# Kernel tuning notes

Measured on AMD Instinct MI355X. Metric: run time of the kernel, lower is better.

The kernel has to match this reference:

```python
import jax, jax.numpy as jnp
import numpy as np

B, S, D, H = 4, 2048, 512, 8
DK = D // H


def setup_inputs() -> dict:
    key = jax.random.key(0)
    ks = jax.random.split(key, 8)
    std = 1.0 / np.sqrt(D)
    return {
        "query": jax.random.normal(ks[0], (B, S, D), jnp.float32),
        "key": jax.random.normal(ks[1], (B, S, D), jnp.float32),
        "value": jax.random.normal(ks[2], (B, S, D), jnp.float32),
        "Wq": jax.random.normal(ks[3], (D, D), jnp.float32) * std,
        "Wk": jax.random.normal(ks[4], (D, D), jnp.float32) * std,
        "Wv": jax.random.normal(ks[5], (D, D), jnp.float32) * std,
        "Wo": jax.random.normal(ks[6], (D, D), jnp.float32) * std,
        "bo": jnp.zeros((D,), jnp.float32),
    }


def reference(query, key, value, Wq, Wk, Wv, Wo, bo):
    # nn.Linear stores weight [out, in]; y = x @ W.T
    def split_heads(x):  # [B,S,D] -> [B,H,S,DK]
        return x.reshape(B, S, H, DK).transpose(0, 2, 1, 3)

    Q = split_heads(query @ Wq.T)
    K = split_heads(key @ Wk.T)
    V = split_heads(value @ Wv.T)
    scale = jnp.sqrt(jnp.asarray(DK, Q.dtype))
    scores = jnp.einsum("bhqd,bhkd->bhqk", Q, K) / scale  # [B,H,S,S]
    attn = jax.nn.softmax(scores, axis=-1)  # dropout=0 / eval mode
    ctx = jnp.einsum("bhqk,bhkd->bhqd", attn, V)
    ctx = ctx.transpose(0, 2, 1, 3).reshape(B, S, D)
    return ctx @ Wo.T + bo
```

## Files before the change

### kernel.cpp

```cpp
#include <hip/hip_runtime.h>
#include <hip/hip_bf16.h>
#include <stdint.h>

#define DEV __device__ __forceinline__

typedef __attribute__((ext_vector_type(8))) __bf16 bf16x8;
typedef __attribute__((ext_vector_type(4))) float f32x4;
typedef __attribute__((ext_vector_type(16))) float f32x16;
typedef __attribute__((ext_vector_type(4))) short short4v;
typedef __attribute__((ext_vector_type(8))) short short8v;
typedef __attribute__((ext_vector_type(4))) unsigned int uint4v;

constexpr int B_ = 4, S_ = 2048, D_ = 512, H_ = 8, DK_ = 64;
constexpr int M_ = B_ * S_;
constexpr int K_ = D_;

DEV unsigned short f2bf(float f) {
  unsigned int u = __builtin_bit_cast(unsigned int, f);
  unsigned int r = (u + 0x7fffu + ((u >> 16) & 1u)) >> 16;
  return (unsigned short)r;
}

DEV void gld16(const void* g, void* l) {
  __builtin_amdgcn_global_load_lds(
      (const __attribute__((address_space(1))) unsigned int*)g,
      (__attribute__((address_space(3))) unsigned int*)l, 16, 0, 0);
}

DEV f32x4 mfma16(bf16x8 a, bf16x8 b, f32x4 c) {
  return __builtin_amdgcn_mfma_f32_16x16x32_bf16(a, b, c, 0, 0, 0);
}
DEV f32x16 mfma32(bf16x8 a, bf16x8 b, f32x16 c) {
  return __builtin_amdgcn_mfma_f32_32x32x16_bf16(a, b, c, 0, 0, 0);
}

DEV short4v tr16(const void* p) {
  short4v d;
  asm volatile("ds_read_b64_tr_b16 %0, %1"
               : "=v"(d)
               : "v"((const __attribute__((address_space(3))) char*)p));
  return d;
}

DEV unsigned pkbf(float a, float b) {
  unsigned r;
  asm("v_cvt_pk_bf16_f32 %0, %1, %2" : "=v"(r) : "v"(a), "v"(b));
  return r;
}

DEV void pl32swap(unsigned& a, unsigned& b) {
  asm volatile("v_permlane32_swap_b32 %0, %1" : "+v"(a), "+v"(b));
}

__global__ __launch_bounds__(256) void convert_all(
    const float* __restrict__ q, const float* __restrict__ k, const float* __restrict__ v,
    const float* __restrict__ wq, const float* __restrict__ wk,
    const float* __restrict__ wv, const float* __restrict__ wo,
    unsigned short* __restrict__ xq, unsigned short* __restrict__ xk,
    unsigned short* __restrict__ xv, unsigned short* __restrict__ wqb,
    unsigned short* __restrict__ wkb, unsigned short* __restrict__ wvb,
    unsigned short* __restrict__ wob)
{
  constexpr int NX = M_ * D_;
  constexpr int NW = D_ * D_;
  constexpr int TOT = (3 * NX + 4 * NW) / 4;
  for (int u = blockIdx.x * blockDim.x + threadIdx.x; u < TOT;
       u += gridDim.x * blockDim.x) {
    int e = u * 4;
    const float* src; unsigned short* dst; int off;
    if (e < 3 * NX) {
      int t = e >> 22; off = e & (NX - 1);
      src = (t == 0) ? q : ((t == 1) ? k : v);
      dst = (t == 0) ? xq : ((t == 1) ? xk : xv);
    } else {
      int e2 = e - 3 * NX;
      int t = e2 >> 18; off = e2 & (NW - 1);
      src = (t == 0) ? wq : ((t == 1) ? wk : ((t == 2) ? wv : wo));
      dst = (t == 0) ? wqb : ((t == 1) ? wkb : ((t == 2) ? wvb : wob));
    }
    float4 f = *(const float4*)(src + off);
    short4v o;
    o.x = (short)f2bf(f.x); o.y = (short)f2bf(f.y);
    o.z = (short)f2bf(f.z); o.w = (short)f2bf(f.w);
    *(short4v*)(dst + off) = o;
  }
}

template <int MODE>
__global__ __launch_bounds__(256, 2) void gemm_bt(
    const unsigned short* __restrict__ A0, const unsigned short* __restrict__ A1,
    const unsigned short* __restrict__ A2,
    const unsigned short* __restrict__ W0, const unsigned short* __restrict__ W1,
    const unsigned short* __restrict__ W2,
    unsigned short* __restrict__ O0, unsigned short* __restrict__ O1,
    unsigned short* __restrict__ O2,
    float* __restrict__ outF, const float* __restrict__ bias)
{
  constexpr int BM = (MODE == 0) ? 128 : 64;
  constexpr int BN = 128, BK = 64, NKT = K_ / BK;
  constexpr int AFR = BM / 32;
  __shared__ unsigned short As[2][BM * BK];
  __shared__ unsigned short Bs[2][BN * BK];
  const int tid = threadIdx.x, lane = tid & 63, wave = tid >> 6;
  const int z = blockIdx.z;
  const unsigned short* A = (MODE == 1 || z == 0) ? A0 : (z == 1 ? A1 : A2);
  const unsigned short* W = (MODE == 1 || z == 0) ? W0 : (z == 1 ? W1 : W2);
  unsigned short* outH = (MODE == 1 || z == 0) ? O0 : (z == 1 ? O1 : O2);
  const int bn0 = blockIdx.x * BN, bm0 = blockIdx.y * BM;
  const int wr = (wave >> 1) * (BM / 2), wc = (wave & 1) * 64;
  const int frow = lane & 15, fk16 = (lane >> 4) * 16;

  f32x4 acc[AFR][4];
#pragma unroll
  for (int i = 0; i < AFR; ++i)
#pragma unroll
    for (int j = 0; j < 4; ++j)
#pragma unroll
      for (int r = 0; r < 4; ++r) acc[i][j][r] = 0.f;

  auto stage = [&](int kt, int buf) {
#pragma unroll
    for (int i = 0; i < BM / 32; ++i) {
      int o = (wave * (BM / 32) + i) * 1024;
      int ol = o + lane * 16;
      int row = ol >> 7, off = (ol ^ ((row & 7) << 4)) & 127;
      gld16((const char*)A + (size_t)(bm0 + row) * (K_ * 2) + kt * 128 + off,
            (char*)As[buf] + o);
    }
#pragma unroll
    for (int i = 0; i < 4; ++i) {
      int o = (wave * 4 + i) * 1024;
      int ol = o + lane * 16;
      int row = ol >> 7, off = (ol ^ ((row & 7) << 4)) & 127;
      gld16((const char*)W + (size_t)(bn0 + row) * (K_ * 2) + kt * 128 + off,
            (char*)Bs[buf] + o);
    }
  };

  stage(0, 0);
  __syncthreads();
  int cur = 0;
  for (int kt = 0; kt < NKT; ++kt) {
    if (kt + 1 < NKT) stage(kt + 1, cur ^ 1);
#pragma unroll
    for (int kc = 0; kc < 2; ++kc) {
      bf16x8 a[AFR], b[4];
#pragma unroll
      for (int i = 0; i < AFR; ++i) {
        int row = wr + i * 16 + frow;
        a[i] = *(const bf16x8*)((const char*)As[cur] +
                ((row * 128 + kc * 64 + fk16) ^ ((row & 7) << 4)));
      }
#pragma unroll
      for (int j = 0; j < 4; ++j) {
        int row = wc + j * 16 + frow;
        b[j] = *(const bf16x8*)((const char*)Bs[cur] +
                ((row * 128 + kc * 64 + fk16) ^ ((row & 7) << 4)));
      }
      __builtin_amdgcn_s_setprio(1);
#pragma unroll
      for (int i = 0; i < AFR; ++i)
#pragma unroll
        for (int j = 0; j < 4; ++j)
          acc[i][j] = mfma16(a[i], b[j], acc[i][j]);
      __builtin_amdgcn_s_setprio(0);
    }
    __syncthreads();
    cur ^= 1;
  }

  const int r0 = (lane >> 4) * 4, cn = lane & 15;
  float bv[4];
  if (MODE == 1) {
#pragma unroll
    for (int j = 0; j < 4; ++j) bv[j] = bias[bn0 + wc + j * 16 + cn];
  }
#pragma unroll
  for (int i = 0; i < AFR; ++i)
#pragma unroll
    for (int j = 0; j < 4; ++j)
#pragma unroll
      for (int r = 0; r < 4; ++r) {
        int gm = bm0 + wr + i * 16 + r0 + r;
        int gn = bn0 + wc + j * 16 + cn;
        float val = acc[i][j][r];
        if (MODE == 0) outH[(size_t)gm * D_ + gn] = f2bf(val);
        else           outF[(size_t)gm * D_ + gn] = val + bv[j];
      }
}

__global__ __launch_bounds__(256, 2) void attn(
    const unsigned short* __restrict__ Qm, const unsigned short* __restrict__ Km,
    const unsigned short* __restrict__ Vm, unsigned short* __restrict__ Ctx)
{
  constexpr int QB = 128, KVB = 64, NT = S_ / KVB;
  __shared__ unsigned short Qs[QB * DK_];
  __shared__ unsigned short Kd[2][KVB * DK_];
  __shared__ unsigned short Vd[2][KVB * DK_];
  __shared__ float smA[4][32];
  const int tid = threadIdx.x, lane = tid & 63, wave = tid >> 6;
  const int hi = lane >> 5, l31 = lane & 31, g1 = (lane >> 4) & 1;
  const int bh = blockIdx.y, q0 = blockIdx.x * QB;
  const int bq = bh >> 3, hh = bh & 7;
  const char* Qg = (const char*)(Qm + ((size_t)bq * S_ + q0) * D_ + hh * DK_);
  const char* Kg = (const char*)(Km + (size_t)bq * S_ * D_ + hh * DK_);
  const char* Vg = (const char*)(Vm + (size_t)bq * S_ * D_ + hh * DK_);

  auto stageSwz = [&](const char* gbase, unsigned short* lds, int o) {
    int ol = o + lane * 16;
    int row = ol >> 7, off = (ol ^ ((row & 7) << 4)) & 127;
    gld16(gbase + (size_t)row * 1024 + off, (char*)lds + o);
  };
  auto stageVt = [&](const char* gbase, unsigned short* lds, int o) {
    int ol = o + lane * 16;
    int E0 = ol >> 1;
    int st = E0 >> 6, rr = (E0 >> 4) & 3, c0 = E0 & 15;
    int kk = (st >> 2) * 4 + rr, dd = (st & 3) * 16 + c0;
    gld16(gbase + (size_t)kk * 1024 + dd * 2, (char*)lds + o);
  };

#pragma unroll
  for (int i = 0; i < 4; ++i) stageSwz(Qg, Qs, (wave * 4 + i) * 1024);
#pragma unroll
  for (int i = 0; i < 2; ++i) stageSwz(Kg, Kd[0], (wave * 2 + i) * 1024);
#pragma unroll
  for (int i = 0; i < 2; ++i) stageVt(Vg, Vd[0], (wave * 2 + i) * 1024);
  __syncthreads();

  bf16x8 qf[4];
  {
    int row = wave * 32 + l31;
    int rb = row * 128, sw = (row & 7) << 4;
#pragma unroll
    for (int c = 0; c < 4; ++c)
      qf[c] = *(const bf16x8*)((const char*)Qs + ((rb + c * 32 + hi * 16) ^ sw));
  }

  f32x16 oacc[2];
#pragma unroll
  for (int dt = 0; dt < 2; ++dt)
#pragma unroll
    for (int r = 0; r < 16; ++r) oacc[dt][r] = 0.f;
  float m2 = -1e30f, lsum = 0.f;
  constexpr float SCL2 = 0.125f * 1.44269504089f;

  int cur = 0;
  for (int t = 0; t < NT; ++t) {
    if (t + 1 < NT) {
      const char* Kg1 = Kg + (size_t)(t + 1) * KVB * 1024;
      const char* Vg1 = Vg + (size_t)(t + 1) * KVB * 1024;
#pragma unroll
      for (int i = 0; i < 2; ++i) stageSwz(Kg1, Kd[cur ^ 1], (wave * 2 + i) * 1024);
#pragma unroll
      for (int i = 0; i < 2; ++i) stageVt(Vg1, Vd[cur ^ 1], (wave * 2 + i) * 1024);
    }

    f32x16 sacc[2];
#pragma unroll
    for (int k2 = 0; k2 < 2; ++k2)
#pragma unroll
      for (int r = 0; r < 16; ++r) sacc[k2][r] = 0.f;
    __builtin_amdgcn_s_setprio(1);
#pragma unroll
    for (int c = 0; c < 4; ++c) {
#pragma unroll
      for (int k2 = 0; k2 < 2; ++k2) {
        int row = k2 * 32 + l31;
        bf16x8 kf = *(const bf16x8*)((const char*)Kd[cur] +
                     ((row * 128 + c * 32 + hi * 16) ^ ((row & 7) << 4)));
        sacc[k2] = mfma32(kf, qf[c], sacc[k2]);
      }
    }
    __builtin_amdgcn_s_setprio(0);

    float mloc = sacc[0][0];
#pragma unroll
    for (int k2 = 0; k2 < 2; ++k2)
#pragma unroll
      for (int r = 0; r < 16; ++r) mloc = fmaxf(mloc, sacc[k2][r]);
    mloc = fmaxf(mloc, __shfl_xor(mloc, 32));
    float m2n = fmaxf(m2, mloc * SCL2);
    float alpha = __builtin_amdgcn_exp2f(m2 - m2n);
    m2 = m2n;
    float psum = 0.f;
#pragma unroll
    for (int k2 = 0; k2 < 2; ++k2)
#pragma unroll
      for (int r = 0; r < 16; ++r) {
        float p = __builtin_amdgcn_exp2f(fmaf(sacc[k2][r], SCL2, -m2n));
        sacc[k2][r] = p;
        psum += p;
      }
    psum += __shfl_xor(psum, 32);
    lsum = lsum * alpha + psum;

    if (lane < 32) smA[wave][lane] = alpha;
    f32x4 av[4];
#pragma unroll
    for (int s = 0; s < 4; ++s)
      av[s] = *(const f32x4*)&smA[wave][s * 8 + hi * 4];
#pragma unroll
    for (int dt = 0; dt < 2; ++dt)
#pragma unroll
      for (int r = 0; r < 16; ++r) oacc[dt][r] *= av[r >> 2][r & 3];

    short4v va[4][2][2];
#pragma unroll
    for (int c = 0; c < 4; ++c)
#pragma unroll
      for (int dt = 0; dt < 2; ++dt) {
        int st = 16 * c + 8 * hi + 2 * dt + g1;
        const char* ad = (const char*)Vd[cur] + st * 128 + (lane & 15) * 8;
        va[c][dt][0] = tr16(ad);
        va[c][dt][1] = tr16(ad + 512);
      }
    bf16x8 pfrag[4];
#pragma unroll
    for (int c = 0; c < 4; ++c) {
      const f32x16& P = sacc[c >> 1];
      const int b = (c & 1) * 8;
      unsigned d0 = pkbf(P[b + 0], P[b + 1]);
      unsigned d1 = pkbf(P[b + 2], P[b + 3]);
      unsigned d2 = pkbf(P[b + 4], P[b + 5]);
      unsigned d3 = pkbf(P[b + 6], P[b + 7]);
      pl32swap(d0, d2);
      pl32swap(d1, d3);
      uint4v pi = {d0, d1, d2, d3};
      pfrag[c] = __builtin_bit_cast(bf16x8, pi);
    }
    asm volatile("s_waitcnt lgkmcnt(0)" ::: "memory");
    __builtin_amdgcn_sched_barrier(0);
    __builtin_amdgcn_s_setprio(1);
#pragma unroll
    for (int c = 0; c < 4; ++c)
#pragma unroll
      for (int dt = 0; dt < 2; ++dt) {
        short8v vv = __builtin_shufflevector(va[c][dt][0], va[c][dt][1],
                                             0, 1, 2, 3, 4, 5, 6, 7);
        oacc[dt] = mfma32(pfrag[c], __builtin_bit_cast(bf16x8, vv), oacc[dt]);
      }
    __builtin_amdgcn_s_setprio(0);

    __syncthreads();
    cur ^= 1;
  }

  if (lane < 32) smA[wave][lane] = 1.f / lsum;
  f32x4 iv[4];
#pragma unroll
  for (int s = 0; s < 4; ++s)
    iv[s] = *(const f32x4*)&smA[wave][s * 8 + hi * 4];
#pragma unroll
  for (int dt = 0; dt < 2; ++dt)
#pragma unroll
    for (int r = 0; r < 16; ++r) {
      int qq = (r & 3) + 8 * (r >> 2) + 4 * hi;
      int grow = q0 + wave * 32 + qq;
      int col = hh * 64 + dt * 32 + l31;
      Ctx[((size_t)bq * S_ + grow) * D_ + col] = f2bf(oacc[dt][r] * iv[r >> 2][r & 3]);
    }
}

extern "C" void kernel_launch(void* const* d_in, const int* in_sizes, int n_in,
                              void* d_out, int out_size, void* d_ws, size_t ws_size,
                              hipStream_t stream) {
  const float* q  = (const float*)d_in[0];
  const float* k  = (const float*)d_in[1];
  const float* v  = (const float*)d_in[2];
  const float* wq = (const float*)d_in[3];
  const float* wk = (const float*)d_in[4];
  const float* wv = (const float*)d_in[5];
  const float* wo = (const float*)d_in[6];
  const float* bo = (const float*)d_in[7];
  float* out = (float*)d_out;

  constexpr size_t NX = (size_t)M_ * D_;
  constexpr size_t NW = (size_t)D_ * D_;
  char* ws = (char*)d_ws;
  unsigned short* Xq  = (unsigned short*)ws; ws += NX * 2;
  unsigned short* Xk  = (unsigned short*)ws; ws += NX * 2;
  unsigned short* Xv  = (unsigned short*)ws; ws += NX * 2;
  unsigned short* Wqb = (unsigned short*)ws; ws += NW * 2;
  unsigned short* Wkb = (unsigned short*)ws; ws += NW * 2;
  unsigned short* Wvb = (unsigned short*)ws; ws += NW * 2;
  unsigned short* Wob = (unsigned short*)ws; ws += NW * 2;
  unsigned short* Qbf = (unsigned short*)ws; ws += NX * 2;
  unsigned short* Kbf = (unsigned short*)ws; ws += NX * 2;
  unsigned short* Vbf = (unsigned short*)ws; ws += NX * 2;
  unsigned short* Cx  = (unsigned short*)ws; ws += NX * 2;

  convert_all<<<2048, 256, 0, stream>>>(q, k, v, wq, wk, wv, wo,
                                        Xq, Xk, Xv, Wqb, Wkb, Wvb, Wob);
  gemm_bt<0><<<dim3(4, 64, 3), 256, 0, stream>>>(
      Xq, Xk, Xv, Wqb, Wkb, Wvb, Qbf, Kbf, Vbf, nullptr, nullptr);
  attn<<<dim3(S_ / 128, B_ * H_), 256, 0, stream>>>(Qbf, Kbf, Vbf, Cx);
  gemm_bt<1><<<dim3(4, 128, 1), 256, 0, stream>>>(
      Cx, nullptr, nullptr, Wob, nullptr, nullptr, nullptr, nullptr, nullptr,
      out, bo);
}
```

Before: 201.9 us.

## Single-buffer GEMM LDS tiles and raise occupancy to 4 blocks per CU

Replaces the double-buffered LDS staging in the projection GEMMs with a single buffer, loaded and synchronised at the top of each K iteration. Per-thread global source addresses are precomputed once, and launch bounds request 4 blocks per CU instead of 2. The aim is to halve LDS use and raise occupancy so other resident blocks hide load latency, at the cost of losing the in-block overlap between loading the next tile and computing the current one. The tighter register budget from the higher occupancy target may also cause spills.

```diff
diff --git a/kernel.cpp b/kernel.cpp
--- a/kernel.cpp
+++ b/kernel.cpp
@@ -87,7 +87,7 @@
 }
 
 template <int MODE>
-__global__ __launch_bounds__(256, 2) void gemm_bt(
+__global__ __launch_bounds__(256, 4) void gemm_bt(
     const unsigned short* __restrict__ A0, const unsigned short* __restrict__ A1,
     const unsigned short* __restrict__ A2,
     const unsigned short* __restrict__ W0, const unsigned short* __restrict__ W1,
@@ -99,8 +99,8 @@
   constexpr int BM = (MODE == 0) ? 128 : 64;
   constexpr int BN = 128, BK = 64, NKT = K_ / BK;
   constexpr int AFR = BM / 32;
-  __shared__ unsigned short As[2][BM * BK];
-  __shared__ unsigned short Bs[2][BN * BK];
+  __shared__ unsigned short As[BM * BK];
+  __shared__ unsigned short Bs[BN * BK];
   const int tid = threadIdx.x, lane = tid & 63, wave = tid >> 6;
   const int z = blockIdx.z;
   const unsigned short* A = (MODE == 1 || z == 0) ? A0 : (z == 1 ? A1 : A2);
@@ -110,6 +110,27 @@
   const int wr = (wave >> 1) * (BM / 2), wc = (wave & 1) * 64;
   const int frow = lane & 15, fk16 = (lane >> 4) * 16;
 
+  const char* srcA[AFR];
+  int dstA[AFR];
+#pragma unroll
+  for (int i = 0; i < AFR; ++i) {
+    int o = (wave * AFR + i) * 1024;
+    int ol = o + lane * 16;
+    int row = ol >> 7, off = (ol ^ ((row & 7) << 4)) & 127;
+    srcA[i] = (const char*)A + (size_t)(bm0 + row) * (K_ * 2) + off;
+    dstA[i] = o;
+  }
+  const char* srcB[4];
+  int dstB[4];
+#pragma unroll
+  for (int i = 0; i < 4; ++i) {
+    int o = (wave * 4 + i) * 1024;
+    int ol = o + lane * 16;
+    int row = ol >> 7, off = (ol ^ ((row & 7) << 4)) & 127;
+    srcB[i] = (const char*)W + (size_t)(bn0 + row) * (K_ * 2) + off;
+    dstB[i] = o;
+  }
+
   f32x4 acc[AFR][4];
 #pragma unroll
   for (int i = 0; i < AFR; ++i)
@@ -118,43 +139,26 @@
 #pragma unroll
       for (int r = 0; r < 4; ++r) acc[i][j][r] = 0.f;
 
-  auto stage = [&](int kt, int buf) {
-#pragma unroll
-    for (int i = 0; i < BM / 32; ++i) {
-      int o = (wave * (BM / 32) + i) * 1024;
-      int ol = o + lane * 16;
-      int row = ol >> 7, off = (ol ^ ((row & 7) << 4)) & 127;
-      gld16((const char*)A + (size_t)(bm0 + row) * (K_ * 2) + kt * 128 + off,
-            (char*)As[buf] + o);
-    }
-#pragma unroll
-    for (int i = 0; i < 4; ++i) {
-      int o = (wave * 4 + i) * 1024;
-      int ol = o + lane * 16;
-      int row = ol >> 7, off = (ol ^ ((row & 7) << 4)) & 127;
-      gld16((const char*)W + (size_t)(bn0 + row) * (K_ * 2) + kt * 128 + off,
-            (char*)Bs[buf] + o);
-    }
-  };
-
-  stage(0, 0);
-  __syncthreads();
-  int cur = 0;
   for (int kt = 0; kt < NKT; ++kt) {
-    if (kt + 1 < NKT) stage(kt + 1, cur ^ 1);
+    __syncthreads();
+#pragma unroll
+    for (int i = 0; i < AFR; ++i) gld16(srcA[i] + kt * 128, (char*)As + dstA[i]);
+#pragma unroll
+    for (int i = 0; i < 4; ++i)   gld16(srcB[i] + kt * 128, (char*)Bs + dstB[i]);
+    __syncthreads();
 #pragma unroll
     for (int kc = 0; kc < 2; ++kc) {
       bf16x8 a[AFR], b[4];
 #pragma unroll
       for (int i = 0; i < AFR; ++i) {
         int row = wr + i * 16 + frow;
-        a[i] = *(const bf16x8*)((const char*)As[cur] +
+        a[i] = *(const bf16x8*)((const char*)As +
                 ((row * 128 + kc * 64 + fk16) ^ ((row & 7) << 4)));
       }
 #pragma unroll
       for (int j = 0; j < 4; ++j) {
         int row = wc + j * 16 + frow;
-        b[j] = *(const bf16x8*)((const char*)Bs[cur] +
+        b[j] = *(const bf16x8*)((const char*)Bs +
                 ((row * 128 + kc * 64 + fk16) ^ ((row & 7) << 4)));
       }
       __builtin_amdgcn_s_setprio(1);
@@ -165,8 +169,6 @@
           acc[i][j] = mfma16(a[i], b[j], acc[i][j]);
       __builtin_amdgcn_s_setprio(0);
     }
-    __syncthreads();
-    cur ^= 1;
   }
 
   const int r0 = (lane >> 4) * 4, cn = lane & 15;
```

Result: no change. 203.1 us (+0.6%).
